# Optimization experiments

Measured on AMD Instinct MI355X. Metric: run time of the kernel, lower is better.

Reference implementation:

```python
import jax, jax.numpy as jnp
import numpy as np

N = 1024   # chain length n
B = 4      # bond_dim (forced by eye(4) bias in original)
P = 2      # phys_dim
BS = 8     # batch size


def setup_inputs() -> dict:
    key = jax.random.key(0)
    k1, k2, k3 = jax.random.split(key, 3)
    data = jax.random.randint(k1, (BS, N), 0, 2).astype(jnp.float32)
    # near-identity init (identity + small noise), as in the original (std*randn + eye bias),
    # but with std large enough to be numerically non-trivial yet stable over ~n matmuls
    eye_b = jnp.eye(B, dtype=jnp.float32)[:, :, None]            # (B, B, 1) broadcast over phys
    tri_up = 0.01 * jax.random.normal(k2, ((N - 1) * N // 2, B, B, P), jnp.float32) + eye_b
    diag = 0.01 * jax.random.normal(k3, (N, B, P), jnp.float32) + 1.0
    return {"data": data, "tri_up": tri_up, "diag": diag}


def reference(data, tri_up, diag):
    bs, n = data.shape
    b = tri_up.shape[1]
    p = tri_up.shape[3]
    emb = jnp.stack([data, 1.0 - data], axis=2)                  # (bs, n, p)
    # scatter tri_up into lower triangle (incl. diagonal) of (n-1, n-1) grid
    r, c = jnp.tril_indices(n - 1)
    T = jnp.zeros((n - 1, n - 1, b, b, p), tri_up.dtype).at[r, c].set(tri_up)
    # contract physical index with embedded spins of sites 0..n-2; output axes swapped to (m, n, bs, b, b)
    T = jnp.einsum('nmlri,bmi->mnblr', T, emb[:, :-1])           # (n-1, n-1, bs, b, b)
    # strict lower triangle (m > n) -> identity matrices
    ru, cu = jnp.triu_indices(n - 1, k=1)
    T = T.at[cu, ru].set(jnp.eye(b, dtype=T.dtype))
    # binary-tree contraction along axis 0 (recursive doubling of 4x4 matmuls)
    size = T.shape[0]
    while size > 1:
        half = size // 2
        nice = 2 * half
        leftover = T[nice:]
        T = jnp.einsum('mnbik,mnbkj->mnbij', T[0:nice:2], T[1:nice:2])
        T = jnp.concatenate([T, leftover], axis=0)
        size = half + (size % 2)
    T = T[0][..., 0, :]                                          # (n-1, bs, b): first row of each matrix
    out = jnp.einsum('nbd,ndp->nbp', T, diag[1:])                # (n-1, bs, p)
    first = jnp.broadcast_to(diag[0, 0], out[0].shape)[None]     # (1, bs, p)
    out = jnp.concatenate([first, out], axis=0)                  # (n, bs, p)
    logx = jax.nn.log_softmax(out, axis=-1).transpose(1, 0, 2)   # (bs, n, p)
    log_prob = logx[:, :, 0] * data + logx[:, :, 1] * (1.0 - data)
    return log_prob.sum(-1)                                      # (bs,)
```

## Files before the change

### kernel.cpp

```cpp
#include <hip/hip_runtime.h>


#define NPOS   1024
#define SEGLEN 64
#define MAXSEG 16
#define CH     8
#define NBUF   4
#define NTASK  8688
#define NWAVE  (NTASK / 2)
#define NBLOCK (NWAVE / 4)
#define TRI_ELEMS (523776 * 32)

template<int l>
__device__ __forceinline__ float qb(float x) {
    constexpr int ctrl = l * 0x55;
    return __int_as_float(__builtin_amdgcn_update_dpp(
        __float_as_int(x), __float_as_int(x), ctrl, 0xF, 0xF, false));
}
template<int ctrl>
__device__ __forceinline__ float qperm(float x) {
    return __int_as_float(__builtin_amdgcn_update_dpp(
        __float_as_int(x), __float_as_int(x), ctrl, 0xF, 0xF, false));
}

__device__ __forceinline__ void gl_lds16(const float* g, float* l) {
    __builtin_amdgcn_global_load_lds(
        (const __attribute__((address_space(1))) void*)g,
        (__attribute__((address_space(3))) void*)l, 16, 0, 0);
}

#define WAITVM(N) __builtin_amdgcn_s_waitcnt((N) | 0x0F70)

__device__ __forceinline__ void decode_task(int id, int& s, int& n) {
    int base = 0, cnt = 1023;
    s = 0;
    while (id >= base + cnt) { base += cnt; s++; cnt -= SEGLEN; }
    n = 1022 - (id - base);
}

__global__ __launch_bounds__(256, 4) void amps_seg(
        const float* __restrict__ data,
        const float* __restrict__ tri,
        float* __restrict__ segout)
{
    const int tid  = threadIdx.x;
    const int wid  = tid >> 6;
    const int lane = tid & 63;
    const int w    = blockIdx.x * 4 + wid;
    const int t    = lane >> 5;
    const int q    = lane & 31;
    const int b    = q >> 2;
    const int i    = q & 3;

    int sA, nA, sB, nB;
    decode_task(2 * w,     sA, nA);
    decode_task(2 * w + 1, sB, nB);
    const int g0A = sA * SEGLEN,            g0B = sB * SEGLEN;
    const int stepsA = min(SEGLEN, nA + 1 - g0A);
    const int stepsB = min(SEGLEN, nB + 1 - g0B);
    const int tstA = (nA * (nA + 1) / 2 + g0A) * 32;
    const int tstB = (nB * (nB + 1) / 2 + g0B) * 32;

    const int fullA = stepsA >> 3,          fullB = stepsB >> 3;
    const int nchA = fullA + ((stepsA & 7) ? 1 : 0);
    const int nchB = fullB + ((stepsB & 7) ? 1 : 0);
    const int nch   = max(nchA, nchB);
    const int mainc = min(fullA, fullB);

    const int g0_my    = t ? g0B : g0A;
    const int steps_my = t ? stepsB : stepsA;
    const int chunkf   = steps_my >> 3;
    const int rem      = steps_my & 7;
    const int n_my     = t ? nB : nA;
    const int s_my     = t ? sB : sA;

    __shared__ float lds_all[4][2][NBUF * CH * 32];
    float* __restrict__ ldsA = &lds_all[wid][0][0];
    float* __restrict__ ldsB = &lds_all[wid][1][0];

    unsigned m0, m1;
    {
        const float4* dp4 = (const float4*)(data + b * NPOS + g0_my + i * 16);
        float4 f0 = dp4[0], f1 = dp4[1], f2 = dp4[2], f3 = dp4[3];
        unsigned piece = 0;
        piece |= (f0.x != 1.0f) ? 1u : 0;        piece |= (f0.y != 1.0f) ? 2u : 0;
        piece |= (f0.z != 1.0f) ? 4u : 0;        piece |= (f0.w != 1.0f) ? 8u : 0;
        piece |= (f1.x != 1.0f) ? 0x10u : 0;     piece |= (f1.y != 1.0f) ? 0x20u : 0;
        piece |= (f1.z != 1.0f) ? 0x40u : 0;     piece |= (f1.w != 1.0f) ? 0x80u : 0;
        piece |= (f2.x != 1.0f) ? 0x100u : 0;    piece |= (f2.y != 1.0f) ? 0x200u : 0;
        piece |= (f2.z != 1.0f) ? 0x400u : 0;    piece |= (f2.w != 1.0f) ? 0x800u : 0;
        piece |= (f3.x != 1.0f) ? 0x1000u : 0;   piece |= (f3.y != 1.0f) ? 0x2000u : 0;
        piece |= (f3.z != 1.0f) ? 0x4000u : 0;   piece |= (f3.w != 1.0f) ? 0x8000u : 0;
        const int sb = t * 32 + b * 4;
        m0 = (unsigned)__shfl((int)piece, sb + 0)
           | ((unsigned)__shfl((int)piece, sb + 1) << 16);
        m1 = (unsigned)__shfl((int)piece, sb + 2)
           | ((unsigned)__shfl((int)piece, sb + 3) << 16);
    }

    auto stageA = [&](int c) {
        int off = min(tstA + c * 256 + lane * 4, TRI_ELEMS - 4);
        gl_lds16(tri + off, ldsA + (c & (NBUF - 1)) * 256);
    };
    auto stageB = [&](int c) {
        int off = min(tstB + c * 256 + lane * 4, TRI_ELEMS - 4);
        gl_lds16(tri + off, ldsB + (c & (NBUF - 1)) * 256);
    };

    stageA(0); stageB(0);
    stageA(1); stageB(1);
    stageA(2); stageB(2);

    float* __restrict__ mybuf = t ? ldsB : ldsA;

    float c0 = (i == 0) ? 1.0f : 0.0f;
    float c1 = (i == 1) ? 1.0f : 0.0f;
    float c2 = (i == 2) ? 1.0f : 0.0f;
    float c3 = (i == 3) ? 1.0f : 0.0f;

    auto bits_of = [&](int c) -> unsigned {
        unsigned word = (c < 4) ? m0 : m1;
        return (word >> ((c & 3) * 8)) & 0xFFu;
    };

    auto compute = [&](int c) {
        const unsigned bits = bits_of(c);
        const float* __restrict__ buf = mybuf + (c & (NBUF - 1)) * 256 + i * 8;
        #pragma unroll
        for (int m = 0; m < CH; m++) {
            const float* p = buf + m * 32 + ((bits >> m) & 1u);
            float a0 = p[0], a1 = p[2], a2 = p[4], a3 = p[6];
            float n0 = qb<0>(a0) * c0;
            n0 = fmaf(qb<1>(a0), c1, n0);
            n0 = fmaf(qb<2>(a0), c2, n0);
            n0 = fmaf(qb<3>(a0), c3, n0);
            float n1 = qb<0>(a1) * c0;
            n1 = fmaf(qb<1>(a1), c1, n1);
            n1 = fmaf(qb<2>(a1), c2, n1);
            n1 = fmaf(qb<3>(a1), c3, n1);
            float n2 = qb<0>(a2) * c0;
            n2 = fmaf(qb<1>(a2), c1, n2);
            n2 = fmaf(qb<2>(a2), c2, n2);
            n2 = fmaf(qb<3>(a2), c3, n2);
            float n3 = qb<0>(a3) * c0;
            n3 = fmaf(qb<1>(a3), c1, n3);
            n3 = fmaf(qb<2>(a3), c2, n3);
            n3 = fmaf(qb<3>(a3), c3, n3);
            c0 = n0; c1 = n1; c2 = n2; c3 = n3;
        }
    };

    int c = 0;
    for (; c < mainc; c++) {
        stageA(c + 3); stageB(c + 3);
        WAITVM(6);
        compute(c);
    }
    const float idval = ((q >> 3) == ((q >> 1) & 3)) ? 1.0f : 0.0f;
    for (; c < nch; c++) {
        stageA(c + 3); stageB(c + 3);
        WAITVM(6);
        if (c >= chunkf) {
            const int mstart = (c == chunkf) ? rem : 0;
            float* bp = mybuf + (c & (NBUF - 1)) * 256 + q;
            for (int m = mstart; m < CH; m++) bp[m * 32] = idval;
        }
        compute(c);
    }

    const size_t o = (((size_t)n_my * MAXSEG + s_my) * 8 + b) * 16 + i;
    segout[o +  0] = c0;
    segout[o +  4] = c1;
    segout[o +  8] = c2;
    segout[o + 12] = c3;
}

__global__ __launch_bounds__(256) void amps_combine(
        const float* __restrict__ segout,
        const float* __restrict__ diag,
        const float* __restrict__ data,
        float* __restrict__ out)
{
    const int tid = threadIdx.x;
    const int q   = tid >> 5;
    const int sub = tid & 31;
    const int b   = sub >> 2;
    const int r   = sub & 3;
    const int n   = blockIdx.x * 8 + q;

    __shared__ float sh[64];

    float res = 0.0f;
    if (n < NPOS - 1) {
        const int nseg = n / SEGLEN + 1;
        const float* basep = segout + (size_t)n * (MAXSEG * 128)
                           + b * 16 + r * 4;
        float v = (r == 0) ? 1.0f : 0.0f;
        #pragma unroll
        for (int s2 = 0; s2 < MAXSEG; s2++) {
            if (s2 >= nseg) break;
            float4 P = *(const float4*)(basep + s2 * 128);
            float acc = qb<0>(v) * P.x;
            acc = fmaf(qb<1>(v), P.y, acc);
            acc = fmaf(qb<2>(v), P.z, acc);
            v   = fmaf(qb<3>(v), P.w, acc);
        }

        const int pos = n + 1;
        const float* dg = diag + pos * 8 + r * 2;
        float o0 = v * dg[0];
        float o1 = v * dg[1];
        o0 += qperm<0xB1>(o0); o0 += qperm<0x4E>(o0);
        o1 += qperm<0xB1>(o1); o1 += qperm<0x4E>(o1);
        float mx  = fmaxf(o0, o1);
        float lse = mx + __logf(__expf(o0 - mx) + __expf(o1 - mx));
        float dsel = data[b * NPOS + pos];
        res = ((dsel == 1.0f) ? o0 : o1) - lse;
    }
    if (r == 0) sh[q * 8 + b] = res;
    __syncthreads();
    if (tid < 8) {
        float ssum = 0.0f;
        #pragma unroll
        for (int qq = 0; qq < 8; qq++) ssum += sh[qq * 8 + tid];
        if (blockIdx.x == 0) {
            float o0 = diag[0], o1 = diag[1];
            float mx  = fmaxf(o0, o1);
            float lse = mx + __logf(__expf(o0 - mx) + __expf(o1 - mx));
            float d0  = data[tid * NPOS];
            ssum += ((d0 == 1.0f) ? o0 : o1) - lse;
        }
        atomicAdd(out + tid, ssum);
    }
}

extern "C" void kernel_launch(void* const* d_in, const int* in_sizes, int n_in,
                              void* d_out, int out_size, void* d_ws, size_t ws_size,
                              hipStream_t stream)
{
    const float* data = (const float*)d_in[0];
    const float* tri  = (const float*)d_in[1];
    const float* diag = (const float*)d_in[2];

    float* segout = (float*)d_ws;
    float* out    = (float*)d_out;

    hipMemsetAsync(d_out, 0, 8 * sizeof(float), stream);
    amps_seg<<<dim3(NBLOCK), dim3(256), 0, stream>>>(data, tri, segout);
    amps_combine<<<dim3(128), dim3(256), 0, stream>>>(segout, diag, data, out);
}
```

Measured before the change: 121.7 us.

## Software-pipeline LDS reads one chunk ahead and merge tail loop

Restructures the segment kernel's inner loop so that LDS reads of the tri matrices rotate through a 4-deep register buffer and are issued ahead of the dependent FMA chain, including a prefetch of the next chunk's first rows. The data load is moved before the async global-to-LDS staging so both are in flight together. The separate main and tail loops become one loop, with identity padding done one chunk ahead and the vmcnt wait relaxed to cover one chunk further. This aims to hide LDS latency in the serial 4x4 matmul chain, at the cost of more registers, a tighter async-load ordering and harder correctness reasoning about buffer reuse.

```diff
diff --git a/kernel.cpp b/kernel.cpp
--- a/kernel.cpp
+++ b/kernel.cpp
@@ -61,11 +61,9 @@
     const int tstA = (nA * (nA + 1) / 2 + g0A) * 32;
     const int tstB = (nB * (nB + 1) / 2 + g0B) * 32;
 
-    const int fullA = stepsA >> 3,          fullB = stepsB >> 3;
-    const int nchA = fullA + ((stepsA & 7) ? 1 : 0);
-    const int nchB = fullB + ((stepsB & 7) ? 1 : 0);
-    const int nch   = max(nchA, nchB);
-    const int mainc = min(fullA, fullB);
+    const int nchA = (stepsA + 7) >> 3;
+    const int nchB = (stepsB + 7) >> 3;
+    const int nch  = max(nchA, nchB);
 
     const int g0_my    = t ? g0B : g0A;
     const int steps_my = t ? stepsB : stepsA;
@@ -77,11 +75,26 @@
     __shared__ float lds_all[4][2][NBUF * CH * 32];
     float* __restrict__ ldsA = &lds_all[wid][0][0];
     float* __restrict__ ldsB = &lds_all[wid][1][0];
+    float* __restrict__ fillbuf = t ? ldsB : ldsA;
+    float* __restrict__ mybuf   = fillbuf + i * 8;
+
+    const float4* dp4 = (const float4*)(data + b * NPOS + g0_my + i * 16);
+    float4 f0 = dp4[0], f1 = dp4[1], f2 = dp4[2], f3 = dp4[3];
+
+    auto stageA = [&](int c) {
+        int off = min(tstA + c * 256 + lane * 4, TRI_ELEMS - 4);
+        gl_lds16(tri + off, ldsA + (c & (NBUF - 1)) * 256);
+    };
+    auto stageB = [&](int c) {
+        int off = min(tstB + c * 256 + lane * 4, TRI_ELEMS - 4);
+        gl_lds16(tri + off, ldsB + (c & (NBUF - 1)) * 256);
+    };
+    stageA(0); stageB(0);
+    stageA(1); stageB(1);
+    stageA(2); stageB(2);
 
     unsigned m0, m1;
     {
-        const float4* dp4 = (const float4*)(data + b * NPOS + g0_my + i * 16);
-        float4 f0 = dp4[0], f1 = dp4[1], f2 = dp4[2], f3 = dp4[3];
         unsigned piece = 0;
         piece |= (f0.x != 1.0f) ? 1u : 0;        piece |= (f0.y != 1.0f) ? 2u : 0;
         piece |= (f0.z != 1.0f) ? 4u : 0;        piece |= (f0.w != 1.0f) ? 8u : 0;
@@ -97,75 +110,75 @@
         m1 = (unsigned)__shfl((int)piece, sb + 2)
            | ((unsigned)__shfl((int)piece, sb + 3) << 16);
     }
-
-    auto stageA = [&](int c) {
-        int off = min(tstA + c * 256 + lane * 4, TRI_ELEMS - 4);
-        gl_lds16(tri + off, ldsA + (c & (NBUF - 1)) * 256);
-    };
-    auto stageB = [&](int c) {
-        int off = min(tstB + c * 256 + lane * 4, TRI_ELEMS - 4);
-        gl_lds16(tri + off, ldsB + (c & (NBUF - 1)) * 256);
-    };
-
-    stageA(0); stageB(0);
-    stageA(1); stageB(1);
-    stageA(2); stageB(2);
-
-    float* __restrict__ mybuf = t ? ldsB : ldsA;
+    auto bits_of = [&](int c) -> unsigned {
+        unsigned word = (c < 4) ? m0 : m1;
+        return (word >> ((c & 3) * 8)) & 0xFFu;
+    };
+
+    const float idval = ((q >> 3) == ((q >> 1) & 3)) ? 1.0f : 0.0f;
+    auto fill = [&](int cc) {
+        const int mstart = (cc == chunkf) ? rem : 0;
+        float* bp = fillbuf + (cc & (NBUF - 1)) * 256 + q;
+        for (int mm = mstart; mm < CH; mm++) bp[mm * 32] = idval;
+    };
+
+    WAITVM(4);
+
+    if (chunkf == 0) fill(0);
 
     float c0 = (i == 0) ? 1.0f : 0.0f;
     float c1 = (i == 1) ? 1.0f : 0.0f;
     float c2 = (i == 2) ? 1.0f : 0.0f;
     float c3 = (i == 3) ? 1.0f : 0.0f;
 
-    auto bits_of = [&](int c) -> unsigned {
-        unsigned word = (c < 4) ? m0 : m1;
-        return (word >> ((c & 3) * 8)) & 0xFFu;
-    };
-
-    auto compute = [&](int c) {
-        const unsigned bits = bits_of(c);
-        const float* __restrict__ buf = mybuf + (c & (NBUF - 1)) * 256 + i * 8;
-        #pragma unroll
-        for (int m = 0; m < CH; m++) {
-            const float* p = buf + m * 32 + ((bits >> m) & 1u);
-            float a0 = p[0], a1 = p[2], a2 = p[4], a3 = p[6];
-            float n0 = qb<0>(a0) * c0;
-            n0 = fmaf(qb<1>(a0), c1, n0);
-            n0 = fmaf(qb<2>(a0), c2, n0);
-            n0 = fmaf(qb<3>(a0), c3, n0);
-            float n1 = qb<0>(a1) * c0;
-            n1 = fmaf(qb<1>(a1), c1, n1);
-            n1 = fmaf(qb<2>(a1), c2, n1);
-            n1 = fmaf(qb<3>(a1), c3, n1);
-            float n2 = qb<0>(a2) * c0;
-            n2 = fmaf(qb<1>(a2), c1, n2);
-            n2 = fmaf(qb<2>(a2), c2, n2);
-            n2 = fmaf(qb<3>(a2), c3, n2);
-            float n3 = qb<0>(a3) * c0;
-            n3 = fmaf(qb<1>(a3), c1, n3);
-            n3 = fmaf(qb<2>(a3), c2, n3);
-            n3 = fmaf(qb<3>(a3), c3, n3);
-            c0 = n0; c1 = n1; c2 = n2; c3 = n3;
-        }
-    };
-
-    int c = 0;
-    for (; c < mainc; c++) {
+    float4 rot[4];
+    auto rd = [&](int cc, int mm, unsigned bits, float4& dst) {
+        const float* p = mybuf + (cc & (NBUF - 1)) * 256 + mm * 32
+                       + ((bits >> mm) & 1u);
+        dst.x = p[0]; dst.y = p[2]; dst.z = p[4]; dst.w = p[6];
+    };
+    auto fmas = [&](const float4& a) {
+        float n0 = qb<0>(a.x) * c0;
+        n0 = fmaf(qb<1>(a.x), c1, n0);
+        n0 = fmaf(qb<2>(a.x), c2, n0);
+        n0 = fmaf(qb<3>(a.x), c3, n0);
+        float n1 = qb<0>(a.y) * c0;
+        n1 = fmaf(qb<1>(a.y), c1, n1);
+        n1 = fmaf(qb<2>(a.y), c2, n1);
+        n1 = fmaf(qb<3>(a.y), c3, n1);
+        float n2 = qb<0>(a.z) * c0;
+        n2 = fmaf(qb<1>(a.z), c1, n2);
+        n2 = fmaf(qb<2>(a.z), c2, n2);
+        n2 = fmaf(qb<3>(a.z), c3, n2);
+        float n3 = qb<0>(a.w) * c0;
+        n3 = fmaf(qb<1>(a.w), c1, n3);
+        n3 = fmaf(qb<2>(a.w), c2, n3);
+        n3 = fmaf(qb<3>(a.w), c3, n3);
+        c0 = n0; c1 = n1; c2 = n2; c3 = n3;
+    };
+
+    unsigned bits_cur = bits_of(0);
+    rd(0, 0, bits_cur, rot[0]);
+    rd(0, 1, bits_cur, rot[1]);
+    rd(0, 2, bits_cur, rot[2]);
+    rd(0, 3, bits_cur, rot[3]);
+
+    for (int c = 0; c < nch; c++) {
         stageA(c + 3); stageB(c + 3);
-        WAITVM(6);
-        compute(c);
-    }
-    const float idval = ((q >> 3) == ((q >> 1) & 3)) ? 1.0f : 0.0f;
-    for (; c < nch; c++) {
-        stageA(c + 3); stageB(c + 3);
-        WAITVM(6);
-        if (c >= chunkf) {
-            const int mstart = (c == chunkf) ? rem : 0;
-            float* bp = mybuf + (c & (NBUF - 1)) * 256 + q;
-            for (int m = mstart; m < CH; m++) bp[m * 32] = idval;
-        }
-        compute(c);
+        WAITVM(4);
+        if (c + 1 >= chunkf && c + 1 < nch) fill(c + 1);
+        const unsigned bits_nxt = bits_of(c + 1);
+
+        fmas(rot[0]); rd(c,     4, bits_cur, rot[0]);
+        fmas(rot[1]); rd(c,     5, bits_cur, rot[1]);
+        fmas(rot[2]); rd(c,     6, bits_cur, rot[2]);
+        fmas(rot[3]); rd(c,     7, bits_cur, rot[3]);
+        fmas(rot[0]); rd(c + 1, 0, bits_nxt, rot[0]);
+        fmas(rot[1]); rd(c + 1, 1, bits_nxt, rot[1]);
+        fmas(rot[2]); rd(c + 1, 2, bits_nxt, rot[2]);
+        fmas(rot[3]); rd(c + 1, 3, bits_nxt, rot[3]);
+
+        bits_cur = bits_nxt;
     }
 
     const size_t o = (((size_t)n_my * MAXSEG + s_my) * 8 + b) * 16 + i;
```

New measurement: 121.7 us. No clear change (+0.1%).
